# Kernel tuning notes

Hardware: AMD Instinct MI355X
Metric: run time of the kernel (lower is better)

Reference implementation:

```python
import jax, jax.numpy as jnp
import numpy as np

TEMPERATURE = 0.1
USE_RANKS = True
USE_SCORES = True
RANK_WEIGHT = 0.1
SCORE_WEIGHT = 0.01
NUM_GROUPS = 1024  # question_ids in [0, NUM_GROUPS)
BATCH = 4096
DIM = 1024


def setup_inputs() -> dict:
    key = jax.random.key(0)
    k1, k2, k3, k4, k5 = jax.random.split(key, 5)
    q_embeddings = jax.random.normal(k1, (BATCH, DIM), dtype=jnp.float32)
    a_embeddings = jax.random.normal(k2, (BATCH, DIM), dtype=jnp.float32)
    question_ids = jax.random.randint(k3, (BATCH,), 0, NUM_GROUPS, dtype=jnp.int32)
    ranks = jax.random.uniform(k4, (BATCH,), dtype=jnp.float32) * 8.0  # ordinal-ish ranks
    scores = jax.random.uniform(k5, (BATCH,), dtype=jnp.float32)
    return {
        "q_embeddings": q_embeddings,
        "a_embeddings": a_embeddings,
        "question_ids": question_ids,
        "ranks": ranks,
        "scores": scores,
    }


def _positive_weights(question_ids, ranks, scores):
    """Per-sample positive weight, normalized to sum to 1 within each question group."""
    w = jnp.ones_like(ranks)
    if USE_RANKS:
        w = w * jnp.exp(-RANK_WEIGHT * ranks)
    if USE_SCORES:
        gmax = jax.ops.segment_max(scores, question_ids, num_segments=NUM_GROUPS)
        gmin = jax.ops.segment_min(scores, question_ids, num_segments=NUM_GROUPS)
        denom = gmax[question_ids] - gmin[question_ids]
        norm = jnp.where(denom > 0, (scores - gmin[question_ids]) / jnp.where(denom > 0, denom, 1.0), 0.0)
        w = w * jnp.exp(SCORE_WEIGHT * norm)
    wsum = jax.ops.segment_sum(w, question_ids, num_segments=NUM_GROUPS)[question_ids]
    gsize = jax.ops.segment_sum(jnp.ones_like(w), question_ids, num_segments=NUM_GROUPS)[question_ids]
    w = jnp.where(wsum > 0, w / jnp.where(wsum > 0, wsum, 1.0), 1.0 / gsize)
    return w


def reference(q_embeddings, a_embeddings, question_ids, ranks, scores):
    B = q_embeddings.shape[0]
    # [B, B] similarity, one fused batched log-softmax over rows
    similarity = jnp.matmul(q_embeddings, a_embeddings.T) / TEMPERATURE
    log_probs = jax.nn.log_softmax(similarity, axis=1)
    # same-group mask: sample j is a positive for row i iff same question id
    same = (question_ids[:, None] == question_ids[None, :])
    w = _positive_weights(question_ids, ranks, scores)  # [B], group-normalized
    # loss_i = -sum_{j in group(i)} w_j * log_probs[i, j]; total averaged over batch
    per_row = -jnp.sum(jnp.where(same, w[None, :] * log_probs, 0.0), axis=1)
    loss = jnp.sum(per_row) / B
    # accuracy: argmax of each row lands inside the row's group
    pred = jnp.argmax(similarity, axis=1)
    acc = jnp.mean((question_ids[pred] == question_ids).astype(jnp.float32))
    return loss, acc
```

## Files before the change

### kernel.cpp

```cpp
#include <hip/hip_runtime.h>
#include <hip/hip_bf16.h>
#include <math.h>

#define BATCH   4096
#define DIM     1024
#define NGROUPS 1024
#define INV_T   10.0f
#define RANK_W  0.1f
#define SCORE_W 0.01f

#define BI 128
#define BJ 256
#define KC 32
#define NT (DIM/KC)
#define NFRAG_Q (BI/16)
#define NFRAG   (BI/16 + BJ/16)
#define NSTG    3
#define FRAG_ELEMS 512

typedef float  floatx4 __attribute__((ext_vector_type(4)));
typedef __bf16 bf16x8  __attribute__((ext_vector_type(8)));
typedef __bf16 bf16x4  __attribute__((ext_vector_type(4)));

#define ASYNC_COPY16(gptr, lptr)                                              \
    __builtin_amdgcn_global_load_lds(                                         \
        (const __attribute__((address_space(1))) void*)(gptr),                \
        (__attribute__((address_space(3))) void*)(lptr), 16, 0, 0)

__global__ __launch_bounds__(256) void prep_kernel(
    const float* __restrict__ Q, const float* __restrict__ A,
    __bf16* __restrict__ Qb, __bf16* __restrict__ Ab,
    const int* __restrict__ qid, const float* __restrict__ ranks,
    const float* __restrict__ scores, float* __restrict__ w)
{
    const int tid = threadIdx.x;

    if (blockIdx.x >= NGROUPS) {
        const int cid = blockIdx.x - NGROUPS;
        const int n4  = BATCH * DIM / 4;
        for (int i = cid * 256 + tid; i < n4; i += 1024 * 256) {
            float4 v = ((const float4*)Q)[i];
            bf16x4 b;
            b[0] = (__bf16)v.x; b[1] = (__bf16)v.y;
            b[2] = (__bf16)v.z; b[3] = (__bf16)v.w;
            ((bf16x4*)Qb)[i] = b;
            v = ((const float4*)A)[i];
            b[0] = (__bf16)v.x; b[1] = (__bf16)v.y;
            b[2] = (__bf16)v.z; b[3] = (__bf16)v.w;
            ((bf16x4*)Ab)[i] = b;
        }
        return;
    }

    const int g = blockIdx.x, lane = tid & 63, wv = tid >> 6;
    __shared__ float rmax[4], rmin[4], rsum[4];

    float gmax = -INFINITY, gmin = INFINITY;
    for (int j = tid; j < BATCH; j += 256) {
        if (qid[j] == g) {
            float s = scores[j];
            gmax = fmaxf(gmax, s);
            gmin = fminf(gmin, s);
        }
    }
    #pragma unroll
    for (int d = 1; d < 64; d <<= 1) {
        gmax = fmaxf(gmax, __shfl_xor(gmax, d, 64));
        gmin = fminf(gmin, __shfl_xor(gmin, d, 64));
    }
    if (lane == 0) { rmax[wv] = gmax; rmin[wv] = gmin; }
    __syncthreads();
    gmax = fmaxf(fmaxf(rmax[0], rmax[1]), fmaxf(rmax[2], rmax[3]));
    gmin = fminf(fminf(rmin[0], rmin[1]), fminf(rmin[2], rmin[3]));
    const float denom     = gmax - gmin;
    const float inv_denom = (denom > 0.f) ? 1.f / denom : 0.f;

    float lsum = 0.f;
    for (int j = tid; j < BATCH; j += 256) {
        if (qid[j] == g) {
            float norm = (scores[j] - gmin) * inv_denom;
            float u = __expf(-RANK_W * ranks[j] + SCORE_W * norm);
            w[j] = u;
            lsum += u;
        }
    }
    #pragma unroll
    for (int d = 1; d < 64; d <<= 1) lsum += __shfl_xor(lsum, d, 64);
    if (lane == 0) rsum[wv] = lsum;
    __syncthreads();
    const float wsum = rsum[0] + rsum[1] + rsum[2] + rsum[3];
    const float inv  = (wsum > 0.f) ? 1.f / wsum : 0.f;
    for (int j = tid; j < BATCH; j += 256) {
        if (qid[j] == g) w[j] *= inv;
    }
}

__global__ __launch_bounds__(512, 4) void fused_simloss_kernel(
    const __bf16* __restrict__ Qb, const __bf16* __restrict__ Ab,
    const int* __restrict__ qid, const float* __restrict__ w,
    float* __restrict__ Pm, float* __restrict__ Pl, float* __restrict__ Ps,
    float* __restrict__ Pbv, int* __restrict__ Pbi)
{
    __shared__ __bf16 sbuf[3][NFRAG * FRAG_ELEMS];

    const int jb = blockIdx.x, ib = blockIdx.y;
    const int i0 = ib * BI, j0 = jb * BJ;
    const int tid = threadIdx.x, wid = tid >> 6, lane = tid & 63;
    const int wm = wid >> 2, wn = wid & 3;
    const int quad = lane >> 4, l16 = lane & 15;

    floatx4 acc[4][4];
    #pragma unroll
    for (int m = 0; m < 4; ++m)
        #pragma unroll
        for (int n = 0; n < 4; ++n)
            #pragma unroll
            for (int c = 0; c < 4; ++c) acc[m][n][c] = 0.f;

    const int lr = lane & 15;
    const int lk = (lane >> 4) * 8;
    const __bf16* src[NSTG];
    #pragma unroll
    for (int c = 0; c < NSTG; ++c) {
        const int f = wid * NSTG + c;
        src[c] = (f < NFRAG_Q)
               ? Qb + (size_t)(i0 + f * 16 + lr) * DIM + lk
               : Ab + (size_t)(j0 + (f - NFRAG_Q) * 16 + lr) * DIM + lk;
    }

    #define STAGE(buf, k0)                                                    \
        do {                                                                  \
            _Pragma("unroll")                                                 \
            for (int c = 0; c < NSTG; ++c)                                    \
                ASYNC_COPY16(src[c] + (k0),                                   \
                             &sbuf[buf][(wid * NSTG + c) * FRAG_ELEMS]);      \
        } while (0)

    STAGE(0, 0);
    STAGE(1, KC);
    STAGE(2, 2 * KC);

    for (int t = 0; t < NT; ++t) {
        if      (t + 2 < NT) asm volatile("s_waitcnt vmcnt(6)\n\ts_barrier" ::: "memory");
        else if (t + 1 < NT) asm volatile("s_waitcnt vmcnt(3)\n\ts_barrier" ::: "memory");
        else                 asm volatile("s_waitcnt vmcnt(0)\n\ts_barrier" ::: "memory");

        const __bf16* cur = sbuf[t % 3];
        bf16x8 qf[4], af[4];
        #pragma unroll
        for (int mf = 0; mf < 4; ++mf)
            qf[mf] = *(const bf16x8*)&cur[(wm * 4 + mf) * FRAG_ELEMS + lane * 8];
        #pragma unroll
        for (int nf = 0; nf < 4; ++nf)
            af[nf] = *(const bf16x8*)&cur[(NFRAG_Q + wn * 4 + nf) * FRAG_ELEMS + lane * 8];

        asm volatile("s_waitcnt lgkmcnt(0)\n\ts_barrier" ::: "memory");
        if (t + 3 < NT) STAGE(t % 3, (t + 3) * KC);

        #pragma unroll
        for (int nf = 0; nf < 4; ++nf)
            #pragma unroll
            for (int mf = 0; mf < 4; ++mf)
                acc[mf][nf] = __builtin_amdgcn_mfma_f32_16x16x32_bf16(
                    qf[mf], af[nf], acc[mf][nf], 0, 0, 0);
    }
    #undef STAGE

    int cq[4]; float cw[4];
    #pragma unroll
    for (int n = 0; n < 4; ++n) {
        int col = j0 + wn * 64 + n * 16 + l16;
        cq[n] = qid[col];
        cw[n] = w[col];
    }
    const int slice = jb * 4 + wn;

    #pragma unroll
    for (int m = 0; m < 4; ++m) {
        #pragma unroll
        for (int reg = 0; reg < 4; ++reg) {
            const int row = i0 + wm * 64 + m * 16 + quad * 4 + reg;
            const int rq  = qid[row];

            float v[4];
            #pragma unroll
            for (int n = 0; n < 4; ++n) v[n] = acc[m][n][reg] * INV_T;

            float lm = fmaxf(fmaxf(v[0], v[1]), fmaxf(v[2], v[3]));
            float ll = __expf(v[0] - lm) + __expf(v[1] - lm) +
                       __expf(v[2] - lm) + __expf(v[3] - lm);
            float ls = 0.f;
            #pragma unroll
            for (int n = 0; n < 4; ++n) ls += (cq[n] == rq) ? cw[n] * v[n] : 0.f;

            float bv = v[0];
            int   bi = j0 + wn * 64 + l16;
            #pragma unroll
            for (int n = 1; n < 4; ++n) {
                int c = j0 + wn * 64 + n * 16 + l16;
                if (v[n] > bv) { bv = v[n]; bi = c; }
            }

            #pragma unroll
            for (int d = 1; d < 16; d <<= 1) {
                float om  = __shfl_xor(lm, d, 64);
                float ol  = __shfl_xor(ll, d, 64);
                float os  = __shfl_xor(ls, d, 64);
                float obv = __shfl_xor(bv, d, 64);
                int   obi = __shfl_xor(bi, d, 64);
                float nm = fmaxf(lm, om);
                ll = ll * __expf(lm - nm) + ol * __expf(om - nm);
                lm = nm;
                ls += os;
                if (obv > bv || (obv == bv && obi < bi)) { bv = obv; bi = obi; }
            }
            if (l16 == 0) {
                int idx = row * 64 + slice;
                Pm[idx] = lm; Pl[idx] = ll; Ps[idx] = ls;
                Pbv[idx] = bv; Pbi[idx] = bi;
            }
        }
    }
}

__global__ __launch_bounds__(256) void row_reduce_kernel(
    const float* __restrict__ Pm, const float* __restrict__ Pl,
    const float* __restrict__ Ps, const float* __restrict__ Pbv,
    const int* __restrict__ Pbi, const int* __restrict__ qid,
    float* __restrict__ per_row, float* __restrict__ ind)
{
    const int r    = blockIdx.x * 4 + (threadIdx.x >> 6);
    const int lane = threadIdx.x & 63;
    const int idx  = r * 64 + lane;

    float m = Pm[idx], l = Pl[idx], s = Ps[idx], bv = Pbv[idx];
    int   bi = Pbi[idx];

    #pragma unroll
    for (int d = 1; d < 64; d <<= 1) {
        float om  = __shfl_xor(m, d, 64);
        float ol  = __shfl_xor(l, d, 64);
        float os  = __shfl_xor(s, d, 64);
        float obv = __shfl_xor(bv, d, 64);
        int   obi = __shfl_xor(bi, d, 64);
        float nm = fmaxf(m, om);
        l = l * __expf(m - nm) + ol * __expf(om - nm);
        m = nm;
        s += os;
        if (obv > bv || (obv == bv && obi < bi)) { bv = obv; bi = obi; }
    }
    if (lane == 0) {
        per_row[r] = (m + logf(l)) - s;
        ind[r]     = (qid[bi] == qid[r]) ? 1.f : 0.f;
    }
}

__global__ __launch_bounds__(1024) void final_kernel(
    const float* __restrict__ per_row, const float* __restrict__ ind,
    float* __restrict__ out)
{
    const int tid = threadIdx.x;
    float s1 = 0.f, s2 = 0.f;
    for (int i = tid; i < BATCH; i += 1024) { s1 += per_row[i]; s2 += ind[i]; }
    #pragma unroll
    for (int d = 1; d < 64; d <<= 1) {
        s1 += __shfl_xor(s1, d, 64);
        s2 += __shfl_xor(s2, d, 64);
    }
    __shared__ float r1[16], r2[16];
    if ((tid & 63) == 0) { r1[tid >> 6] = s1; r2[tid >> 6] = s2; }
    __syncthreads();
    if (tid == 0) {
        float t1 = 0.f, t2 = 0.f;
        #pragma unroll
        for (int i = 0; i < 16; ++i) { t1 += r1[i]; t2 += r2[i]; }
        out[0] = t1 / (float)BATCH;
        out[1] = t2 / (float)BATCH;
    }
}

extern "C" void kernel_launch(void* const* d_in, const int* in_sizes, int n_in,
                              void* d_out, int out_size, void* d_ws, size_t ws_size,
                              hipStream_t stream)
{
    const float* Q      = (const float*)d_in[0];
    const float* A      = (const float*)d_in[1];
    const int*   qid    = (const int*)d_in[2];
    const float* ranks  = (const float*)d_in[3];
    const float* scores = (const float*)d_in[4];
    float* out = (float*)d_out;

    __bf16* Qb = (__bf16*)d_ws;
    __bf16* Ab = Qb + (size_t)BATCH * DIM;
    float* w       = (float*)(Ab + (size_t)BATCH * DIM);
    float* Pm      = w + BATCH;
    float* Pl      = Pm + BATCH * 64;
    float* Ps      = Pl + BATCH * 64;
    float* Pbv     = Ps + BATCH * 64;
    int*   Pbi     = (int*)(Pbv + BATCH * 64);
    float* per_row = (float*)(Pbi + BATCH * 64);
    float* ind     = per_row + BATCH;

    prep_kernel<<<2048, 256, 0, stream>>>(Q, A, Qb, Ab, qid, ranks, scores, w);

    dim3 grid(BATCH / BJ, BATCH / BI);
    fused_simloss_kernel<<<grid, 512, 0, stream>>>(Qb, Ab, qid, w, Pm, Pl, Ps, Pbv, Pbi);

    row_reduce_kernel<<<BATCH / 4, 256, 0, stream>>>(Pm, Pl, Ps, Pbv, Pbi, qid, per_row, ind);

    final_kernel<<<1, 1024, 0, stream>>>(per_row, ind, out);
}
```

Measured before the change: 163.3 us.

## Rework LDS pipeline to one barrier per step and simplify softmax shuffle reduce

The main K loop now keeps two loads in flight instead of three and rotates three LDS buffer pointers. The next stage is issued right after a single barrier, which removes the second lgkmcnt barrier each iteration, and the MFMA block runs at raised wave priority via s_setprio. In the epilogue, the row max is reduced across 16 lanes first, so the sum-of-exp reduction becomes plain adds and the per-step exp rescaling goes away. The cost is a shallower prefetch depth, which may expose more global-load latency.

Measured after the change: 157.0 us. -3.9%, faster.

```diff
diff --git a/kernel.cpp b/kernel.cpp
--- a/kernel.cpp
+++ b/kernel.cpp
@@ -128,24 +128,28 @@
                : Ab + (size_t)(j0 + (f - NFRAG_Q) * 16 + lr) * DIM + lk;
     }
 
-    #define STAGE(buf, k0)                                                    \
+    #define STAGE(bufptr, k0)                                                 \
         do {                                                                  \
             _Pragma("unroll")                                                 \
             for (int c = 0; c < NSTG; ++c)                                    \
                 ASYNC_COPY16(src[c] + (k0),                                   \
-                             &sbuf[buf][(wid * NSTG + c) * FRAG_ELEMS]);      \
+                             (__bf16*)(bufptr) + (wid * NSTG + c) * FRAG_ELEMS); \
         } while (0)
 
-    STAGE(0, 0);
-    STAGE(1, KC);
-    STAGE(2, 2 * KC);
+    __bf16* bprev = sbuf[2];
+    __bf16* bcur  = sbuf[0];
+    __bf16* bnext = sbuf[1];
+
+    STAGE(bcur, 0);
+    STAGE(bnext, KC);
 
     for (int t = 0; t < NT; ++t) {
-        if      (t + 2 < NT) asm volatile("s_waitcnt vmcnt(6)\n\ts_barrier" ::: "memory");
-        else if (t + 1 < NT) asm volatile("s_waitcnt vmcnt(3)\n\ts_barrier" ::: "memory");
-        else                 asm volatile("s_waitcnt vmcnt(0)\n\ts_barrier" ::: "memory");
-
-        const __bf16* cur = sbuf[t % 3];
+        if (t < NT - 1) asm volatile("s_waitcnt vmcnt(3)\n\ts_barrier" ::: "memory");
+        else            asm volatile("s_waitcnt vmcnt(0)\n\ts_barrier" ::: "memory");
+
+        if (t + 2 < NT) STAGE(bprev, (t + 2) * KC);
+
+        const __bf16* cur = bcur;
         bf16x8 qf[4], af[4];
         #pragma unroll
         for (int mf = 0; mf < 4; ++mf)
@@ -154,15 +158,17 @@
         for (int nf = 0; nf < 4; ++nf)
             af[nf] = *(const bf16x8*)&cur[(NFRAG_Q + wn * 4 + nf) * FRAG_ELEMS + lane * 8];
 
-        asm volatile("s_waitcnt lgkmcnt(0)\n\ts_barrier" ::: "memory");
-        if (t + 3 < NT) STAGE(t % 3, (t + 3) * KC);
-
+        __builtin_amdgcn_s_setprio(1);
         #pragma unroll
         for (int nf = 0; nf < 4; ++nf)
             #pragma unroll
             for (int mf = 0; mf < 4; ++mf)
                 acc[mf][nf] = __builtin_amdgcn_mfma_f32_16x16x32_bf16(
                     qf[mf], af[nf], acc[mf][nf], 0, 0, 0);
+        __builtin_amdgcn_s_setprio(0);
+
+        __bf16* tmp = bprev;
+        bprev = bcur; bcur = bnext; bnext = tmp;
     }
     #undef STAGE
 
@@ -186,9 +192,13 @@
             #pragma unroll
             for (int n = 0; n < 4; ++n) v[n] = acc[m][n][reg] * INV_T;
 
-            float lm = fmaxf(fmaxf(v[0], v[1]), fmaxf(v[2], v[3]));
-            float ll = __expf(v[0] - lm) + __expf(v[1] - lm) +
-                       __expf(v[2] - lm) + __expf(v[3] - lm);
+            float pm = fmaxf(fmaxf(v[0], v[1]), fmaxf(v[2], v[3]));
+            #pragma unroll
+            for (int d = 1; d < 16; d <<= 1)
+                pm = fmaxf(pm, __shfl_xor(pm, d, 64));
+
+            float ll = __expf(v[0] - pm) + __expf(v[1] - pm) +
+                       __expf(v[2] - pm) + __expf(v[3] - pm);
             float ls = 0.f;
             #pragma unroll
             for (int n = 0; n < 4; ++n) ls += (cq[n] == rq) ? cw[n] * v[n] : 0.f;
@@ -203,20 +213,15 @@
 
             #pragma unroll
             for (int d = 1; d < 16; d <<= 1) {
-                float om  = __shfl_xor(lm, d, 64);
-                float ol  = __shfl_xor(ll, d, 64);
-                float os  = __shfl_xor(ls, d, 64);
+                ll += __shfl_xor(ll, d, 64);
+                ls += __shfl_xor(ls, d, 64);
                 float obv = __shfl_xor(bv, d, 64);
                 int   obi = __shfl_xor(bi, d, 64);
-                float nm = fmaxf(lm, om);
-                ll = ll * __expf(lm - nm) + ol * __expf(om - nm);
-                lm = nm;
-                ls += os;
                 if (obv > bv || (obv == bv && obi < bi)) { bv = obv; bi = obi; }
             }
             if (l16 == 0) {
                 int idx = row * 64 + slice;
-                Pm[idx] = lm; Pl[idx] = ll; Ps[idx] = ls;
+                Pm[idx] = pm; Pl[idx] = ll; Ps[idx] = ls;
                 Pbv[idx] = bv; Pbi[idx] = bi;
             }
         }
```
